# Performance work log

Hardware: AMD Instinct MI355X
Metric: run time of the kernel (lower is better)

Reference implementation:

```python
import jax, jax.numpy as jnp
import numpy as np

WS = 8            # window size
N = WS * WS       # tokens per window
C = 192           # in_features
H = 6             # heads
HD = C // H       # head dim
MH = 256          # meta network hidden
BW = 4096         # batch_size * windows
NW_MASK = 64      # number of mask window patterns


def _relative_coords_log():
    idx = np.arange(WS)
    coords = np.stack(np.meshgrid(idx, idx, indexing='ij'), axis=0).reshape(2, -1)  # [2, N]
    rel = coords[:, :, None] - coords[:, None, :]            # [2, N, N]
    rel = rel.transpose(1, 2, 0).reshape(-1, 2).astype(np.float32)  # [N*N, 2]
    return jnp.asarray(np.sign(rel) * np.log1p(np.abs(rel)))


def setup_inputs() -> dict:
    key = jax.random.key(0)
    ks = jax.random.split(key, 12)
    s = 0.02
    return {
        'x': jax.random.normal(ks[0], (BW, C, WS, WS), jnp.float32),
        'mask': jax.random.normal(ks[1], (NW_MASK, N, N), jnp.float32),
        'W_qkv': jax.random.normal(ks[2], (C, 3 * C), jnp.float32) * s,
        'b_qkv': jnp.zeros((3 * C,), jnp.float32),
        'W_proj': jax.random.normal(ks[3], (C, C), jnp.float32) * s,
        'b_proj': jnp.zeros((C,), jnp.float32),
        'mW1': jax.random.normal(ks[4], (2, MH), jnp.float32) * 0.1,
        'mb1': jnp.zeros((MH,), jnp.float32),
        'mW2': jax.random.normal(ks[5], (MH, H), jnp.float32) * 0.1,
        'mb2': jnp.zeros((H,), jnp.float32),
        'tau': jnp.ones((H,), jnp.float32),
    }


def _l2norm(v):
    n = jnp.sqrt(jnp.sum(v * v, axis=-1, keepdims=True))
    return v / jnp.maximum(n, 1e-12)


def reference(x, mask, W_qkv, b_qkv, W_proj, b_proj, mW1, mb1, mW2, mb2, tau):
    Bw = x.shape[0]
    # [Bw, C, ws, ws] -> tokens [Bw, N, C]
    tokens = x.reshape(Bw, C, N).transpose(0, 2, 1)
    qkv = tokens @ W_qkv + b_qkv                                  # [Bw, N, 3C]
    qkv = qkv.reshape(Bw, N, 3, H, HD).transpose(2, 0, 3, 1, 4)   # [3, Bw, H, N, HD]
    q, k, v = qkv[0], qkv[1], qkv[2]
    # scaled cosine attention
    attn = jnp.einsum('bhnd,bhmd->bhnm', _l2norm(q), _l2norm(k))
    attn = attn / jnp.clip(tau, 0.01, None)[None, :, None, None]
    # continuous relative position bias via meta network
    rel_log = _relative_coords_log()                              # [N*N, 2]
    bias = jax.nn.relu(rel_log @ mW1 + mb1) @ mW2 + mb2           # [N*N, H]
    bias = bias.T.reshape(H, N, N)
    attn = attn + bias[None]
    # shifted-window mask, pattern indexed by window id modulo nW_mask
    idx = jnp.arange(Bw) % mask.shape[0]
    attn = attn + mask[idx][:, None]                              # [Bw, 1, N, N]
    attn = jax.nn.softmax(attn, axis=-1)
    out = jnp.einsum('bhnm,bhmd->bhnd', attn, v)
    out = out.transpose(0, 2, 1, 3).reshape(Bw, N, C)
    out = out @ W_proj + b_proj
    # back to [Bw, C, ws, ws]
    return out.transpose(0, 2, 1).reshape(Bw, C, WS, WS)
```

## Files before the change

kernel.cpp:

```cpp
#include <hip/hip_runtime.h>

typedef _Float16 f16;
typedef _Float16 f16x2 __attribute__((ext_vector_type(2)));
typedef _Float16 f16x4 __attribute__((ext_vector_type(4)));
typedef _Float16 f16x8 __attribute__((ext_vector_type(8)));
typedef float f32x4 __attribute__((ext_vector_type(4)));

#define NT 64
#define CH 192
#define NH 6
#define MH 256
#define BWIN 4096
#define LOG2E 1.44269504f

#define STOK 200
#define SMEM_FUSED 49152

#define MFMA16(a, b, c) __builtin_amdgcn_mfma_f32_16x16x16f16(a, b, c, 0, 0, 0)
#define MFMA32(a, b, c) __builtin_amdgcn_mfma_f32_16x16x32_f16(a, b, c, 0, 0, 0)

__device__ __forceinline__ int qkidx(int n, int d) {
    return n * 32 + ((((d >> 3) + (n >> 1)) & 3) << 3) + (d & 7);
}

__global__ void bias_kernel(const float* __restrict__ mW1, const float* __restrict__ mb1,
                            const float* __restrict__ mW2, const float* __restrict__ mb2,
                            float* __restrict__ bias_tbl) {
    int p = blockIdx.x * blockDim.x + threadIdx.x;
    if (p >= NT * NT) return;
    int n = p >> 6, m = p & 63;
    float di = (float)((n >> 3) - (m >> 3));
    float dj = (float)((n & 7) - (m & 7));
    float r0 = copysignf(log1pf(fabsf(di)), di);
    float r1 = copysignf(log1pf(fabsf(dj)), dj);
    float acc[NH];
#pragma unroll
    for (int h = 0; h < NH; h++) acc[h] = mb2[h];
    for (int k = 0; k < MH; k++) {
        float hv = fmaxf(r0 * mW1[k] + r1 * mW1[MH + k] + mb1[k], 0.0f);
#pragma unroll
        for (int h = 0; h < NH; h++) acc[h] += hv * mW2[k * NH + h];
    }
#pragma unroll
    for (int h = 0; h < NH; h++) bias_tbl[h * (NT * NT) + p] = acc[h];
}

__global__ void prep_kernel(const float* __restrict__ Wqkv, const float* __restrict__ Wproj,
                            f16* __restrict__ Wpk, f16* __restrict__ Wpp) {
    int i = blockIdx.x * blockDim.x + threadIdx.x;
    const int NQ = 36 * 6 * 64 * 8;
    if (i < NQ) {
        int t = i & 7, lane = (i >> 3) & 63, ks = (i >> 9) % 6, ct = i >> 9; ct /= 6;
        int o = 16 * ct + (lane & 15);
        int c = ks * 32 + (lane >> 4) * 8 + t;
        Wpk[i] = (f16)Wqkv[c * 576 + o];
    } else if (i < NQ + 12 * 6 * 64 * 8) {
        int j = i - NQ;
        int t = j & 7, lane = (j >> 3) & 63, ks = (j >> 9) % 6, ct = j >> 9; ct /= 6;
        int o = 16 * ct + (lane & 15);
        int c = ks * 32 + (lane >> 4) * 8 + t;
        Wpp[j] = (f16)Wproj[c * 192 + o];
    }
}

__global__ void comb_kernel(const float* __restrict__ mask, const float* __restrict__ bias_tbl,
                            float* __restrict__ comb) {
    int j = blockIdx.x * blockDim.x + threadIdx.x;
    if (j >= 64 * NH * NT * NT) return;
    int im = j / (NH * NT * NT);
    int rem = j % (NH * NT * NT);
    int h = rem >> 12;
    int p = rem & 4095;
    comb[j] = (mask[im * 4096 + p] + bias_tbl[h * 4096 + p]) * LOG2E;
}

__launch_bounds__(384, 1)
__global__ void qkv_kernel(const float* __restrict__ x, const float* __restrict__ bqkv,
                           const f16* __restrict__ Wpk, f16* __restrict__ qkv_ws) {
    __shared__ __align__(16) f16 tok[NT * STOK];

    const int tid = threadIdx.x;
    const int l   = tid & 63;
    const int w   = __builtin_amdgcn_readfirstlane(tid >> 6);
    const int b   = blockIdx.x;
    const int c16 = l & 15;
    const int g4  = l >> 4;

    {
        const float* xb = x + (size_t)b * (CH * NT);
        const int n4 = 4 * c16;
#pragma unroll
        for (int i = 0; i < 4; i++) {
            int c = 32 * w + 8 * g4 + 2 * i;
            f32x4 a0 = *(const f32x4*)(xb + c * NT + n4);
            f32x4 a1 = *(const f32x4*)(xb + (c + 1) * NT + n4);
#pragma unroll
            for (int j = 0; j < 4; j++) {
                f16x2 p;
                p[0] = (f16)a0[j];
                p[1] = (f16)a1[j];
                *(f16x2*)(tok + (n4 + j) * STOK + c) = p;
            }
        }
    }
    __syncthreads();

    f16* dstq = qkv_ws + (size_t)(b * NH + w) * 6144;
    f16* dstk = dstq + 2048;
    f16* dstv = dstq + 4096;

    {
        f16x8 wf[6][2];
#pragma unroll
        for (int ks = 0; ks < 6; ks++)
#pragma unroll
            for (int dt = 0; dt < 2; dt++)
                wf[ks][dt] = *(const f16x8*)(Wpk + (((size_t)(2 * w + dt) * 6 + ks) * 64 + l) * 8);
        f32x4 acc[2][4] = {};
#pragma unroll
        for (int ks = 0; ks < 6; ks++) {
            f16x8 af[4];
#pragma unroll
            for (int nt = 0; nt < 4; nt++)
                af[nt] = *(const f16x8*)(tok + (16 * nt + c16) * STOK + ks * 32 + 8 * g4);
#pragma unroll
            for (int dt = 0; dt < 2; dt++)
#pragma unroll
                for (int nt = 0; nt < 4; nt++)
                    acc[dt][nt] = MFMA32(wf[ks][dt], af[nt], acc[dt][nt]);
        }
        f32x4 bb0 = *(const f32x4*)(bqkv + 32 * w + 4 * g4);
        f32x4 bb1 = *(const f32x4*)(bqkv + 32 * w + 16 + 4 * g4);
#pragma unroll
        for (int nt = 0; nt < 4; nt++) {
            float a0[4], a1[4];
            float ss = 0.f;
#pragma unroll
            for (int r = 0; r < 4; r++) {
                a0[r] = acc[0][nt][r] + bb0[r];
                a1[r] = acc[1][nt][r] + bb1[r];
                ss += a0[r] * a0[r] + a1[r] * a1[r];
            }
            ss += __shfl_xor(ss, 16);
            ss += __shfl_xor(ss, 32);
            float inv = 1.0f / fmaxf(sqrtf(ss), 1e-12f);
            f16x4 h0, h1;
#pragma unroll
            for (int r = 0; r < 4; r++) {
                h0[r] = (f16)(a0[r] * inv);
                h1[r] = (f16)(a1[r] * inv);
            }
            *(f16x4*)(dstq + (16 * nt + c16) * 32 + 4 * g4)      = h0;
            *(f16x4*)(dstq + (16 * nt + c16) * 32 + 16 + 4 * g4) = h1;
        }
    }
    {
        f16x8 wf[6][2];
#pragma unroll
        for (int ks = 0; ks < 6; ks++)
#pragma unroll
            for (int dt = 0; dt < 2; dt++)
                wf[ks][dt] = *(const f16x8*)(Wpk + (((size_t)(12 + 2 * w + dt) * 6 + ks) * 64 + l) * 8);
        f32x4 acc[2][4] = {};
#pragma unroll
        for (int ks = 0; ks < 6; ks++) {
            f16x8 af[4];
#pragma unroll
            for (int nt = 0; nt < 4; nt++)
                af[nt] = *(const f16x8*)(tok + (16 * nt + c16) * STOK + ks * 32 + 8 * g4);
#pragma unroll
            for (int dt = 0; dt < 2; dt++)
#pragma unroll
                for (int nt = 0; nt < 4; nt++)
                    acc[dt][nt] = MFMA32(wf[ks][dt], af[nt], acc[dt][nt]);
        }
        f32x4 bb0 = *(const f32x4*)(bqkv + CH + 32 * w + 4 * g4);
        f32x4 bb1 = *(const f32x4*)(bqkv + CH + 32 * w + 16 + 4 * g4);
#pragma unroll
        for (int nt = 0; nt < 4; nt++) {
            float a0[4], a1[4];
            float ss = 0.f;
#pragma unroll
            for (int r = 0; r < 4; r++) {
                a0[r] = acc[0][nt][r] + bb0[r];
                a1[r] = acc[1][nt][r] + bb1[r];
                ss += a0[r] * a0[r] + a1[r] * a1[r];
            }
            ss += __shfl_xor(ss, 16);
            ss += __shfl_xor(ss, 32);
            float inv = 1.0f / fmaxf(sqrtf(ss), 1e-12f);
            f16x4 h0, h1;
#pragma unroll
            for (int r = 0; r < 4; r++) {
                h0[r] = (f16)(a0[r] * inv);
                h1[r] = (f16)(a1[r] * inv);
            }
            *(f16x4*)(dstk + (16 * nt + c16) * 32 + 4 * g4)      = h0;
            *(f16x4*)(dstk + (16 * nt + c16) * 32 + 16 + 4 * g4) = h1;
        }
    }
    {
        f16x8 wf[6][2];
#pragma unroll
        for (int ks = 0; ks < 6; ks++)
#pragma unroll
            for (int dt = 0; dt < 2; dt++)
                wf[ks][dt] = *(const f16x8*)(Wpk + (((size_t)(24 + 2 * w + dt) * 6 + ks) * 64 + l) * 8);
        f32x4 acc[2][4] = {};
#pragma unroll
        for (int ks = 0; ks < 6; ks++) {
            f16x8 af[4];
#pragma unroll
            for (int mt = 0; mt < 4; mt++)
                af[mt] = *(const f16x8*)(tok + (16 * mt + c16) * STOK + ks * 32 + 8 * g4);
#pragma unroll
            for (int dt = 0; dt < 2; dt++)
#pragma unroll
                for (int mt = 0; mt < 4; mt++)
                    acc[dt][mt] = MFMA32(af[mt], wf[ks][dt], acc[dt][mt]);
        }
#pragma unroll
        for (int dt = 0; dt < 2; dt++) {
            float bb = bqkv[384 + 32 * w + 16 * dt + c16];
#pragma unroll
            for (int mt = 0; mt < 4; mt++) {
                f16x4 h;
#pragma unroll
                for (int r = 0; r < 4; r++) h[r] = (f16)(acc[dt][mt][r] + bb);
                *(f16x4*)(dstv + ((dt * 4 + mt) * 64 + l) * 4) = h;
            }
        }
    }
}

__launch_bounds__(384, 1)
__global__ void attn2_kernel(const float* __restrict__ tau, const f16* __restrict__ Wpp,
                             const float* __restrict__ bproj, const float* __restrict__ comb,
                             const f16* __restrict__ qkv_ws, float* __restrict__ out) {
    __shared__ __align__(16) f16 ao[NT * STOK];

    const int tid = threadIdx.x;
    const int l   = tid & 63;
    const int w   = __builtin_amdgcn_readfirstlane(tid >> 6);
    const int b   = blockIdx.x;
    const int c16 = l & 15;
    const int g4  = l >> 4;

    const f16* qg = qkv_ws + (size_t)(b * NH + w) * 6144;
    const f16* kg = qg + 2048;
    const f16* vg = qg + 4096;

    f16x4 vb[2][4];
#pragma unroll
    for (int dt = 0; dt < 2; dt++)
#pragma unroll
        for (int mk = 0; mk < 4; mk++)
            vb[dt][mk] = *(const f16x4*)(vg + ((dt * 4 + mk) * 64 + l) * 4);
    f16x8 wpp[6][2];
#pragma unroll
    for (int ks = 0; ks < 6; ks++)
#pragma unroll
        for (int c2 = 0; c2 < 2; c2++)
            wpp[ks][c2] = *(const f16x8*)(Wpp + (((size_t)(2 * w + c2) * 6 + ks) * 64 + l) * 8);

    const float itau_l2 = LOG2E / fmaxf(tau[w], 0.01f);
    const float* cb = comb + ((size_t)((b & 63) * NH + w)) * (NT * NT);

#pragma unroll
    for (int half = 0; half < 2; half++) {
        f32x4 cc[4][2];
#pragma unroll
        for (int mt = 0; mt < 4; mt++)
#pragma unroll
            for (int ntl = 0; ntl < 2; ntl++)
                cc[mt][ntl] = *(const f32x4*)(cb + (16 * (2 * half + ntl) + c16) * NT + 16 * mt + 4 * g4);

        f16x8 aqf[2];
#pragma unroll
        for (int ntl = 0; ntl < 2; ntl++)
            aqf[ntl] = *(const f16x8*)(qg + (16 * (2 * half + ntl) + c16) * 32 + 8 * g4);
        f16x8 akf[4];
#pragma unroll
        for (int mt = 0; mt < 4; mt++)
            akf[mt] = *(const f16x8*)(kg + (16 * mt + c16) * 32 + 8 * g4);

        f32x4 sv[4][2];
#pragma unroll
        for (int mt = 0; mt < 4; mt++)
#pragma unroll
            for (int ntl = 0; ntl < 2; ntl++) {
                f32x4 z = {};
                sv[mt][ntl] = MFMA32(akf[mt], aqf[ntl], z);
            }
#pragma unroll
        for (int mt = 0; mt < 4; mt++)
#pragma unroll
            for (int ntl = 0; ntl < 2; ntl++)
#pragma unroll
                for (int r = 0; r < 4; r++)
                    sv[mt][ntl][r] = sv[mt][ntl][r] * itau_l2 + cc[mt][ntl][r];
#pragma unroll
        for (int ntl = 0; ntl < 2; ntl++) {
            float mx = sv[0][ntl][0];
#pragma unroll
            for (int mt = 0; mt < 4; mt++)
#pragma unroll
                for (int r = 0; r < 4; r++) mx = fmaxf(mx, sv[mt][ntl][r]);
            mx = fmaxf(mx, __shfl_xor(mx, 16));
            mx = fmaxf(mx, __shfl_xor(mx, 32));
            float sum = 0.f;
#pragma unroll
            for (int mt = 0; mt < 4; mt++)
#pragma unroll
                for (int r = 0; r < 4; r++) {
                    float p = exp2f(sv[mt][ntl][r] - mx);
                    sv[mt][ntl][r] = p;
                    sum += p;
                }
            sum += __shfl_xor(sum, 16);
            sum += __shfl_xor(sum, 32);
            float ris = 1.0f / sum;
#pragma unroll
            for (int mt = 0; mt < 4; mt++)
#pragma unroll
                for (int r = 0; r < 4; r++) sv[mt][ntl][r] *= ris;
        }
        f16x4 pa[4][2];
#pragma unroll
        for (int mk = 0; mk < 4; mk++)
#pragma unroll
            for (int ntl = 0; ntl < 2; ntl++) {
                f16x4 h;
#pragma unroll
                for (int r = 0; r < 4; r++) h[r] = (f16)sv[mk][ntl][r];
                pa[mk][ntl] = h;
            }
        f32x4 av[2][2] = {};
#pragma unroll
        for (int mk = 0; mk < 4; mk++)
#pragma unroll
            for (int ntl = 0; ntl < 2; ntl++)
#pragma unroll
                for (int dt = 0; dt < 2; dt++)
                    av[ntl][dt] = MFMA16(pa[mk][ntl], vb[dt][mk], av[ntl][dt]);
#pragma unroll
        for (int ntl = 0; ntl < 2; ntl++)
#pragma unroll
            for (int dt = 0; dt < 2; dt++)
#pragma unroll
                for (int r = 0; r < 4; r++)
                    ao[(16 * (2 * half + ntl) + 4 * g4 + r) * STOK + 32 * w + 16 * dt + c16] =
                        (f16)av[ntl][dt][r];
    }
    __syncthreads();

    f32x4 acc2[2][4] = {};
#pragma unroll
    for (int ks = 0; ks < 6; ks++) {
        f16x8 af[4];
#pragma unroll
        for (int rt = 0; rt < 4; rt++)
            af[rt] = *(const f16x8*)(ao + (16 * rt + c16) * STOK + ks * 32 + 8 * g4);
#pragma unroll
        for (int c2 = 0; c2 < 2; c2++)
#pragma unroll
            for (int rt = 0; rt < 4; rt++)
                acc2[c2][rt] = MFMA32(af[rt], wpp[ks][c2], acc2[c2][rt]);
    }
    float* ob = out + (size_t)b * (CH * NT);
#pragma unroll
    for (int c2 = 0; c2 < 2; c2++) {
        int c = 16 * (2 * w + c2) + c16;
        float bp = bproj[c];
#pragma unroll
        for (int rt = 0; rt < 4; rt++) {
            f32x4 o4 = acc2[c2][rt];
            o4[0] += bp; o4[1] += bp; o4[2] += bp; o4[3] += bp;
            *(f32x4*)(ob + c * NT + 16 * rt + 4 * g4) = o4;
        }
    }
}

__launch_bounds__(384)
__global__ void attn_fused_kernel(const float* __restrict__ x, const float* __restrict__ bqkv,
                                  const float* __restrict__ bproj, const float* __restrict__ tau,
                                  const f16* __restrict__ Wpk, const f16* __restrict__ Wpp,
                                  const float* __restrict__ comb, float* __restrict__ out) {
    __shared__ __align__(16) char smem[SMEM_FUSED];
    f16* tok = (f16*)smem;
    f16* qk  = (f16*)smem;
    f16* ao  = (f16*)smem;

    const int b   = blockIdx.x;
    const int tid = threadIdx.x;
    const int l   = tid & 63;
    const int w   = __builtin_amdgcn_readfirstlane(tid >> 6);
    const int c16 = l & 15;
    const int g4  = l >> 4;

    {
        const float* xb = x + (size_t)b * (CH * NT);
        const int n4 = 4 * c16;
#pragma unroll
        for (int i = 0; i < 4; i++) {
            int c = 32 * w + 8 * g4 + 2 * i;
            f32x4 a0 = *(const f32x4*)(xb + c * NT + n4);
            f32x4 a1 = *(const f32x4*)(xb + (c + 1) * NT + n4);
#pragma unroll
            for (int j = 0; j < 4; j++) {
                f16x2 p;
                p[0] = (f16)a0[j];
                p[1] = (f16)a1[j];
                *(f16x2*)(tok + (n4 + j) * STOK + c) = p;
            }
        }
    }
    __syncthreads();

    f16x4 hq[2][4], hk[2][4];
    {
        f32x4 aq_[2][4] = {};
#pragma unroll
        for (int ks = 0; ks < 6; ks++) {
            f16x8 af[4];
#pragma unroll
            for (int nt = 0; nt < 4; nt++)
                af[nt] = *(const f16x8*)(tok + (16 * nt + c16) * STOK + ks * 32 + 8 * g4);
#pragma unroll
            for (int dt = 0; dt < 2; dt++) {
                f16x8 wf = *(const f16x8*)(Wpk + (((size_t)(2 * w + dt) * 6 + ks) * 64 + l) * 8);
#pragma unroll
                for (int nt = 0; nt < 4; nt++)
                    aq_[dt][nt] = MFMA32(wf, af[nt], aq_[dt][nt]);
            }
        }
#pragma unroll
        for (int dt = 0; dt < 2; dt++) {
            f32x4 bb = *(const f32x4*)(bqkv + 32 * w + 16 * dt + 4 * g4);
#pragma unroll
            for (int nt = 0; nt < 4; nt++)
#pragma unroll
                for (int r = 0; r < 4; r++) aq_[dt][nt][r] += bb[r];
        }
#pragma unroll
        for (int nt = 0; nt < 4; nt++) {
            float ss = 0.f;
#pragma unroll
            for (int dt = 0; dt < 2; dt++)
#pragma unroll
                for (int r = 0; r < 4; r++) ss += aq_[dt][nt][r] * aq_[dt][nt][r];
            ss += __shfl_xor(ss, 16);
            ss += __shfl_xor(ss, 32);
            float iq = 1.0f / fmaxf(sqrtf(ss), 1e-12f);
#pragma unroll
            for (int dt = 0; dt < 2; dt++)
#pragma unroll
                for (int r = 0; r < 4; r++) hq[dt][nt][r] = (f16)(aq_[dt][nt][r] * iq);
        }
    }
    {
        f32x4 ak_[2][4] = {};
// ... 145 lines not shown
#pragma unroll
    for (int mk = 0; mk < 4; mk++)
#pragma unroll
        for (int nt = 0; nt < 4; nt++)
#pragma unroll
            for (int dt = 0; dt < 2; dt++)
                av[nt][dt] = MFMA16(pa[mk][nt], vb[dt][mk], av[nt][dt]);

    __syncthreads();
#pragma unroll
    for (int nt = 0; nt < 4; nt++)
#pragma unroll
        for (int dt = 0; dt < 2; dt++)
#pragma unroll
            for (int r = 0; r < 4; r++)
                ao[(16 * nt + 4 * g4 + r) * STOK + 32 * w + 16 * dt + c16] = (f16)av[nt][dt][r];
    __syncthreads();

    f32x4 acc2[2][4] = {};
#pragma unroll
    for (int ks = 0; ks < 6; ks++) {
        f16x8 af[4];
#pragma unroll
        for (int rt = 0; rt < 4; rt++)
            af[rt] = *(const f16x8*)(ao + (16 * rt + c16) * STOK + ks * 32 + 8 * g4);
#pragma unroll
        for (int c2 = 0; c2 < 2; c2++) {
            f16x8 bw = *(const f16x8*)(Wpp + (((size_t)(2 * w + c2) * 6 + ks) * 64 + l) * 8);
#pragma unroll
            for (int rt = 0; rt < 4; rt++)
                acc2[c2][rt] = MFMA32(af[rt], bw, acc2[c2][rt]);
        }
    }
    float* ob = out + (size_t)b * (CH * NT);
#pragma unroll
    for (int c2 = 0; c2 < 2; c2++) {
        int c = 16 * (2 * w + c2) + c16;
        float bp = bproj[c];
#pragma unroll
        for (int rt = 0; rt < 4; rt++) {
            f32x4 o4 = acc2[c2][rt];
            o4[0] += bp; o4[1] += bp; o4[2] += bp; o4[3] += bp;
            *(f32x4*)(ob + c * NT + 16 * rt + 4 * g4) = o4;
        }
    }
}

#define WS_BIAS 0
#define WS_WPK  98304
#define WS_WPP  319488
#define WS_COMB 393216
#define WS_QKV  6684672
#define WS_NEED ((size_t)WS_QKV + (size_t)BWIN * NH * 6144 * 2)

extern "C" void kernel_launch(void* const* d_in, const int* in_sizes, int n_in,
                              void* d_out, int out_size, void* d_ws, size_t ws_size,
                              hipStream_t stream) {
    const float* x     = (const float*)d_in[0];
    const float* mask  = (const float*)d_in[1];
    const float* Wqkv  = (const float*)d_in[2];
    const float* bqkv  = (const float*)d_in[3];
    const float* Wproj = (const float*)d_in[4];
    const float* bproj = (const float*)d_in[5];
    const float* mW1   = (const float*)d_in[6];
    const float* mb1   = (const float*)d_in[7];
    const float* mW2   = (const float*)d_in[8];
    const float* mb2   = (const float*)d_in[9];
    const float* tau   = (const float*)d_in[10];

    char* ws = (char*)d_ws;
    float* bias_tbl = (float*)(ws + WS_BIAS);
    f16*   Wpk      = (f16*)(ws + WS_WPK);
    f16*   Wpp      = (f16*)(ws + WS_WPP);
    float* comb     = (float*)(ws + WS_COMB);
    f16*   qkv_ws   = (f16*)(ws + WS_QKV);

    bias_kernel<<<16, 256, 0, stream>>>(mW1, mb1, mW2, mb2, bias_tbl);
    int prep_n = 36 * 6 * 64 * 8 + 12 * 6 * 64 * 8;
    prep_kernel<<<(prep_n + 255) / 256, 256, 0, stream>>>(Wqkv, Wproj, Wpk, Wpp);
    int comb_n = 64 * NH * NT * NT;
    comb_kernel<<<(comb_n + 255) / 256, 256, 0, stream>>>(mask, bias_tbl, comb);

    if (ws_size >= WS_NEED) {
        qkv_kernel<<<BWIN, 384, 0, stream>>>(x, bqkv, Wpk, qkv_ws);
        attn2_kernel<<<BWIN, 384, 0, stream>>>(tau, Wpp, bproj, comb, qkv_ws, (float*)d_out);
    } else {
        attn_fused_kernel<<<BWIN, 384, 0, stream>>>(x, bqkv, bproj, tau, Wpk, Wpp, comb,
                                                    (float*)d_out);
    }
}
```

Before: 314.5 us.

## Stage weights and QKV tiles through LDS with async global-to-LDS loads

Replaces per-lane register preloads of the packed QKV and projection weights and the per-window q/k/v tiles with asynchronous global_load_lds transfers into shared-memory staging buffers. In the QKV kernel the next weight slice is prefetched during each epilogue, and q/k are written with an XOR swizzle that the attention kernel reads back. V is now stored in wider 8-element vectors, and the attention output staging buffer reuses the q/k/v staging area after a barrier. This is meant to cut register pressure and overlap weight fetch with compute, at the cost of a much larger shared-memory footprint that may limit occupancy, plus hand-placed wait counters.

```diff
diff --git a/kernel.cpp b/kernel.cpp
--- a/kernel.cpp
+++ b/kernel.cpp
@@ -18,6 +18,16 @@
 
 #define MFMA16(a, b, c) __builtin_amdgcn_mfma_f32_16x16x16f16(a, b, c, 0, 0, 0)
 #define MFMA32(a, b, c) __builtin_amdgcn_mfma_f32_16x16x32_f16(a, b, c, 0, 0, 0)
+
+typedef const __attribute__((address_space(1))) void* gas_ptr;
+typedef __attribute__((address_space(3))) void* las_ptr;
+__device__ __forceinline__ void gload_lds16(const void* g, void* l) {
+    __builtin_amdgcn_global_load_lds((gas_ptr)g, (las_ptr)l, 16, 0, 0);
+}
+#define WAIT_VMCNT(N) do { asm volatile("s_waitcnt vmcnt(" #N ")" ::: "memory"); \
+                           __builtin_amdgcn_sched_barrier(0); } while (0)
+#define WAIT_LGKM0()  do { asm volatile("s_waitcnt lgkmcnt(0)" ::: "memory"); \
+                           __builtin_amdgcn_sched_barrier(0); } while (0)
 
 __device__ __forceinline__ int qkidx(int n, int d) {
     return n * 32 + ((((d >> 3) + (n >> 1)) & 3) << 3) + (d & 7);
@@ -78,6 +88,7 @@
 __global__ void qkv_kernel(const float* __restrict__ x, const float* __restrict__ bqkv,
                            const f16* __restrict__ Wpk, f16* __restrict__ qkv_ws) {
     __shared__ __align__(16) f16 tok[NT * STOK];
+    __shared__ __align__(16) f16 wstage[6 * 6144];
 
     const int tid = threadIdx.x;
     const int l   = tid & 63;
@@ -86,6 +97,15 @@
     const int c16 = l & 15;
     const int g4  = l >> 4;
 
+    f16* wbuf = wstage + w * 6144;
+
+    {
+        const f16* src = Wpk + (size_t)(2 * w) * 3072;
+#pragma unroll
+        for (int j = 0; j < 12; j++)
+            gload_lds16(src + j * 512 + l * 8, wbuf + j * 512);
+    }
+
     {
         const float* xb = x + (size_t)b * (CH * NT);
         const int n4 = 4 * c16;
@@ -104,31 +124,37 @@
         }
     }
     __syncthreads();
-
+    WAIT_VMCNT(0);
+
+    const int swz = ((c16 >> 1) & 3) << 3;
     f16* dstq = qkv_ws + (size_t)(b * NH + w) * 6144;
     f16* dstk = dstq + 2048;
     f16* dstv = dstq + 4096;
 
     {
-        f16x8 wf[6][2];
-#pragma unroll
-        for (int ks = 0; ks < 6; ks++)
-#pragma unroll
-            for (int dt = 0; dt < 2; dt++)
-                wf[ks][dt] = *(const f16x8*)(Wpk + (((size_t)(2 * w + dt) * 6 + ks) * 64 + l) * 8);
         f32x4 acc[2][4] = {};
 #pragma unroll
         for (int ks = 0; ks < 6; ks++) {
+            f16x8 wf0 = *(const f16x8*)(wbuf + (ks * 64 + l) * 8);
+            f16x8 wf1 = *(const f16x8*)(wbuf + ((6 + ks) * 64 + l) * 8);
             f16x8 af[4];
 #pragma unroll
             for (int nt = 0; nt < 4; nt++)
                 af[nt] = *(const f16x8*)(tok + (16 * nt + c16) * STOK + ks * 32 + 8 * g4);
 #pragma unroll
-            for (int dt = 0; dt < 2; dt++)
-#pragma unroll
-                for (int nt = 0; nt < 4; nt++)
-                    acc[dt][nt] = MFMA32(wf[ks][dt], af[nt], acc[dt][nt]);
-        }
+            for (int nt = 0; nt < 4; nt++) {
+                acc[0][nt] = MFMA32(wf0, af[nt], acc[0][nt]);
+                acc[1][nt] = MFMA32(wf1, af[nt], acc[1][nt]);
+            }
+        }
+        WAIT_LGKM0();
+        {
+            const f16* src = Wpk + (size_t)(12 + 2 * w) * 3072;
+#pragma unroll
+            for (int j = 0; j < 12; j++)
+                gload_lds16(src + j * 512 + l * 8, wbuf + j * 512);
+        }
+        __builtin_amdgcn_sched_barrier(0);
         f32x4 bb0 = *(const f32x4*)(bqkv + 32 * w + 4 * g4);
         f32x4 bb1 = *(const f32x4*)(bqkv + 32 * w + 16 + 4 * g4);
 #pragma unroll
@@ -150,30 +176,37 @@
                 h0[r] = (f16)(a0[r] * inv);
                 h1[r] = (f16)(a1[r] * inv);
             }
-            *(f16x4*)(dstq + (16 * nt + c16) * 32 + 4 * g4)      = h0;
-            *(f16x4*)(dstq + (16 * nt + c16) * 32 + 16 + 4 * g4) = h1;
-        }
-    }
-    {
-        f16x8 wf[6][2];
-#pragma unroll
-        for (int ks = 0; ks < 6; ks++)
-#pragma unroll
-            for (int dt = 0; dt < 2; dt++)
-                wf[ks][dt] = *(const f16x8*)(Wpk + (((size_t)(12 + 2 * w + dt) * 6 + ks) * 64 + l) * 8);
+            int base = (16 * nt + c16) * 32;
+            *(f16x4*)(dstq + base + ((4 * g4) ^ swz))      = h0;
+            *(f16x4*)(dstq + base + ((16 + 4 * g4) ^ swz)) = h1;
+        }
+    }
+    WAIT_VMCNT(0);
+
+    {
         f32x4 acc[2][4] = {};
 #pragma unroll
         for (int ks = 0; ks < 6; ks++) {
+            f16x8 wf0 = *(const f16x8*)(wbuf + (ks * 64 + l) * 8);
+            f16x8 wf1 = *(const f16x8*)(wbuf + ((6 + ks) * 64 + l) * 8);
             f16x8 af[4];
 #pragma unroll
             for (int nt = 0; nt < 4; nt++)
                 af[nt] = *(const f16x8*)(tok + (16 * nt + c16) * STOK + ks * 32 + 8 * g4);
 #pragma unroll
-            for (int dt = 0; dt < 2; dt++)
-#pragma unroll
-                for (int nt = 0; nt < 4; nt++)
-                    acc[dt][nt] = MFMA32(wf[ks][dt], af[nt], acc[dt][nt]);
-        }
+            for (int nt = 0; nt < 4; nt++) {
+                acc[0][nt] = MFMA32(wf0, af[nt], acc[0][nt]);
+                acc[1][nt] = MFMA32(wf1, af[nt], acc[1][nt]);
+            }
+        }
+        WAIT_LGKM0();
+        {
+            const f16* src = Wpk + (size_t)(24 + 2 * w) * 3072;
+#pragma unroll
+            for (int j = 0; j < 12; j++)
+                gload_lds16(src + j * 512 + l * 8, wbuf + j * 512);
+        }
+        __builtin_amdgcn_sched_barrier(0);
         f32x4 bb0 = *(const f32x4*)(bqkv + CH + 32 * w + 4 * g4);
         f32x4 bb1 = *(const f32x4*)(bqkv + CH + 32 * w + 16 + 4 * g4);
 #pragma unroll
@@ -195,40 +228,45 @@
                 h0[r] = (f16)(a0[r] * inv);
                 h1[r] = (f16)(a1[r] * inv);
             }
-            *(f16x4*)(dstk + (16 * nt + c16) * 32 + 4 * g4)      = h0;
-            *(f16x4*)(dstk + (16 * nt + c16) * 32 + 16 + 4 * g4) = h1;
-        }
-    }
-    {
-        f16x8 wf[6][2];
-#pragma unroll
-        for (int ks = 0; ks < 6; ks++)
-#pragma unroll
-            for (int dt = 0; dt < 2; dt++)
-                wf[ks][dt] = *(const f16x8*)(Wpk + (((size_t)(24 + 2 * w + dt) * 6 + ks) * 64 + l) * 8);
+            int base = (16 * nt + c16) * 32;
+            *(f16x4*)(dstk + base + ((4 * g4) ^ swz))      = h0;
+            *(f16x4*)(dstk + base + ((16 + 4 * g4) ^ swz)) = h1;
+        }
+    }
+    WAIT_VMCNT(0);
+
+    {
         f32x4 acc[2][4] = {};
 #pragma unroll
         for (int ks = 0; ks < 6; ks++) {
+            f16x8 wf0 = *(const f16x8*)(wbuf + (ks * 64 + l) * 8);
+            f16x8 wf1 = *(const f16x8*)(wbuf + ((6 + ks) * 64 + l) * 8);
             f16x8 af[4];
 #pragma unroll
             for (int mt = 0; mt < 4; mt++)
                 af[mt] = *(const f16x8*)(tok + (16 * mt + c16) * STOK + ks * 32 + 8 * g4);
 #pragma unroll
-            for (int dt = 0; dt < 2; dt++)
-#pragma unroll
-                for (int mt = 0; mt < 4; mt++)
-                    acc[dt][mt] = MFMA32(af[mt], wf[ks][dt], acc[dt][mt]);
-        }
+            for (int mt = 0; mt < 4; mt++) {
+                acc[0][mt] = MFMA32(af[mt], wf0, acc[0][mt]);
+                acc[1][mt] = MFMA32(af[mt], wf1, acc[1][mt]);
+            }
+        }
+        f16x4 hv[2][4];
 #pragma unroll
         for (int dt = 0; dt < 2; dt++) {
             float bb = bqkv[384 + 32 * w + 16 * dt + c16];
 #pragma unroll
-            for (int mt = 0; mt < 4; mt++) {
-                f16x4 h;
-#pragma unroll
-                for (int r = 0; r < 4; r++) h[r] = (f16)(acc[dt][mt][r] + bb);
-                *(f16x4*)(dstv + ((dt * 4 + mt) * 64 + l) * 4) = h;
-            }
+            for (int mt = 0; mt < 4; mt++)
+#pragma unroll
+                for (int r = 0; r < 4; r++) hv[dt][mt][r] = (f16)(acc[dt][mt][r] + bb);
+        }
+#pragma unroll
+        for (int p = 0; p < 4; p++) {
+            int dt = p >> 1, m0 = 2 * (p & 1);
+            f16x8 v8;
+#pragma unroll
+            for (int r = 0; r < 4; r++) { v8[r] = hv[dt][m0][r]; v8[4 + r] = hv[dt][m0 + 1][r]; }
+            *(f16x8*)(dstv + (p * 64 + l) * 8) = v8;
         }
     }
 }
@@ -237,7 +275,8 @@
 __global__ void attn2_kernel(const float* __restrict__ tau, const f16* __restrict__ Wpp,
                              const float* __restrict__ bproj, const float* __restrict__ comb,
                              const f16* __restrict__ qkv_ws, float* __restrict__ out) {
-    __shared__ __align__(16) f16 ao[NT * STOK];
+    __shared__ __align__(16) f16 qkvstage[6 * 6144];
+    __shared__ __align__(16) f16 wppstage[6 * 6144];
 
     const int tid = threadIdx.x;
     const int l   = tid & 63;
@@ -246,26 +285,37 @@
     const int c16 = l & 15;
     const int g4  = l >> 4;
 
-    const f16* qg = qkv_ws + (size_t)(b * NH + w) * 6144;
-    const f16* kg = qg + 2048;
-    const f16* vg = qg + 4096;
-
-    f16x4 vb[2][4];
-#pragma unroll
-    for (int dt = 0; dt < 2; dt++)
-#pragma unroll
-        for (int mk = 0; mk < 4; mk++)
-            vb[dt][mk] = *(const f16x4*)(vg + ((dt * 4 + mk) * 64 + l) * 4);
-    f16x8 wpp[6][2];
-#pragma unroll
-    for (int ks = 0; ks < 6; ks++)
-#pragma unroll
-        for (int c2 = 0; c2 < 2; c2++)
-            wpp[ks][c2] = *(const f16x8*)(Wpp + (((size_t)(2 * w + c2) * 6 + ks) * 64 + l) * 8);
+    f16* Lq = qkvstage + w * 6144;
+    f16* Lw = wppstage + w * 6144;
+    f16* ao = qkvstage;
+
+    {
+        const f16* srcq = qkv_ws + (size_t)(b * NH + w) * 6144;
+#pragma unroll
+        for (int j = 0; j < 12; j++)
+            gload_lds16(srcq + j * 512 + l * 8, Lq + j * 512);
+        const f16* srcw = Wpp + (size_t)(2 * w) * 3072;
+#pragma unroll
+        for (int j = 0; j < 12; j++)
+            gload_lds16(srcw + j * 512 + l * 8, Lw + j * 512);
+    }
 
     const float itau_l2 = LOG2E / fmaxf(tau[w], 0.01f);
     const float* cb = comb + ((size_t)((b & 63) * NH + w)) * (NT * NT);
-
+    const int swz = ((c16 >> 1) & 3) << 3;
+
+    WAIT_VMCNT(12);
+
+    f16x4 vb[2][4];
+#pragma unroll
+    for (int p = 0; p < 4; p++) {
+        f16x8 v8 = *(const f16x8*)(Lq + 4096 + (p * 64 + l) * 8);
+        int dt = p >> 1, m0 = 2 * (p & 1);
+#pragma unroll
+        for (int r = 0; r < 4; r++) { vb[dt][m0][r] = v8[r]; vb[dt][m0 + 1][r] = v8[4 + r]; }
+    }
+
+    f32x4 avh[2][2][2];
 #pragma unroll
     for (int half = 0; half < 2; half++) {
         f32x4 cc[4][2];
@@ -278,11 +328,11 @@
         f16x8 aqf[2];
 #pragma unroll
         for (int ntl = 0; ntl < 2; ntl++)
-            aqf[ntl] = *(const f16x8*)(qg + (16 * (2 * half + ntl) + c16) * 32 + 8 * g4);
+            aqf[ntl] = *(const f16x8*)(Lq + (16 * (2 * half + ntl) + c16) * 32 + ((8 * g4) ^ swz));
         f16x8 akf[4];
 #pragma unroll
         for (int mt = 0; mt < 4; mt++)
-            akf[mt] = *(const f16x8*)(kg + (16 * mt + c16) * 32 + 8 * g4);
+            akf[mt] = *(const f16x8*)(Lq + 2048 + (16 * mt + c16) * 32 + ((8 * g4) ^ swz));
 
         f32x4 sv[4][2];
 #pragma unroll
@@ -347,12 +397,23 @@
         for (int ntl = 0; ntl < 2; ntl++)
 #pragma unroll
             for (int dt = 0; dt < 2; dt++)
+                avh[half][ntl][dt] = av[ntl][dt];
+    }
+
+    __syncthreads();
+
+#pragma unroll
+    for (int half = 0; half < 2; half++)
+#pragma unroll
+        for (int ntl = 0; ntl < 2; ntl++)
+#pragma unroll
+            for (int dt = 0; dt < 2; dt++)
 #pragma unroll
                 for (int r = 0; r < 4; r++)
                     ao[(16 * (2 * half + ntl) + 4 * g4 + r) * STOK + 32 * w + 16 * dt + c16] =
-                        (f16)av[ntl][dt][r];
-    }
+                        (f16)avh[half][ntl][dt][r];
     __syncthreads();
+    WAIT_VMCNT(0);
 
     f32x4 acc2[2][4] = {};
 #pragma unroll
@@ -361,11 +422,13 @@
 #pragma unroll
         for (int rt = 0; rt < 4; rt++)
             af[rt] = *(const f16x8*)(ao + (16 * rt + c16) * STOK + ks * 32 + 8 * g4);
-#pragma unroll
-        for (int c2 = 0; c2 < 2; c2++)
-#pragma unroll
-            for (int rt = 0; rt < 4; rt++)
-                acc2[c2][rt] = MFMA32(af[rt], wpp[ks][c2], acc2[c2][rt]);
+        f16x8 w0 = *(const f16x8*)(Lw + (ks * 64 + l) * 8);
+        f16x8 w1 = *(const f16x8*)(Lw + ((6 + ks) * 64 + l) * 8);
+#pragma unroll
+        for (int rt = 0; rt < 4; rt++) {
+            acc2[0][rt] = MFMA32(af[rt], w0, acc2[0][rt]);
+            acc2[1][rt] = MFMA32(af[rt], w1, acc2[1][rt]);
+        }
     }
     float* ob = out + (size_t)b * (CH * NT);
 #pragma unroll
```

Measured after the change: 380.8 us. 1.21x slower.

## Process two windows per block in QKV and attention kernels

Applied to the files above, without the earlier changes.

Each block of the QKV and attention kernels now handles two windows instead of one, with doubled LDS buffers and grids halved. The weight fragments held in registers are reused across both windows, and interleaving two independent MFMA chains gives more instruction-level parallelism. The V layout is also packed into 16-byte stores and loads. The cost is roughly double register and LDS pressure per block and half as many blocks, which may reduce occupancy or cause spills.

```diff
diff --git a/kernel.cpp b/kernel.cpp
--- a/kernel.cpp
+++ b/kernel.cpp
@@ -74,40 +74,73 @@
     comb[j] = (mask[im * 4096 + p] + bias_tbl[h * 4096 + p]) * LOG2E;
 }
 
+__device__ __forceinline__ void norm_store(const f32x4 (&acc)[2][4], const float* __restrict__ bq,
+                                           int c16, int g4, f16* __restrict__ dst) {
+    f32x4 bb0 = *(const f32x4*)(bq + 4 * g4);
+    f32x4 bb1 = *(const f32x4*)(bq + 16 + 4 * g4);
+#pragma unroll
+    for (int nt = 0; nt < 4; nt++) {
+        float a0[4], a1[4];
+        float ss = 0.f;
+#pragma unroll
+        for (int r = 0; r < 4; r++) {
+            a0[r] = acc[0][nt][r] + bb0[r];
+            a1[r] = acc[1][nt][r] + bb1[r];
+            ss += a0[r] * a0[r] + a1[r] * a1[r];
+        }
+        ss += __shfl_xor(ss, 16);
+        ss += __shfl_xor(ss, 32);
+        float inv = 1.0f / fmaxf(sqrtf(ss), 1e-12f);
+        f16x4 h0, h1;
+#pragma unroll
+        for (int r = 0; r < 4; r++) {
+            h0[r] = (f16)(a0[r] * inv);
+            h1[r] = (f16)(a1[r] * inv);
+        }
+        *(f16x4*)(dst + (16 * nt + c16) * 32 + 4 * g4)      = h0;
+        *(f16x4*)(dst + (16 * nt + c16) * 32 + 16 + 4 * g4) = h1;
+    }
+}
+
 __launch_bounds__(384, 1)
 __global__ void qkv_kernel(const float* __restrict__ x, const float* __restrict__ bqkv,
                            const f16* __restrict__ Wpk, f16* __restrict__ qkv_ws) {
-    __shared__ __align__(16) f16 tok[NT * STOK];
+    __shared__ __align__(16) f16 tokA[NT * STOK];
+    __shared__ __align__(16) f16 tokB[NT * STOK];
 
     const int tid = threadIdx.x;
     const int l   = tid & 63;
     const int w   = __builtin_amdgcn_readfirstlane(tid >> 6);
-    const int b   = blockIdx.x;
+    const int b0  = blockIdx.x * 2;
+    const int b1  = b0 + 1;
     const int c16 = l & 15;
     const int g4  = l >> 4;
 
     {
-        const float* xb = x + (size_t)b * (CH * NT);
         const int n4 = 4 * c16;
 #pragma unroll
-        for (int i = 0; i < 4; i++) {
-            int c = 32 * w + 8 * g4 + 2 * i;
-            f32x4 a0 = *(const f32x4*)(xb + c * NT + n4);
-            f32x4 a1 = *(const f32x4*)(xb + (c + 1) * NT + n4);
-#pragma unroll
-            for (int j = 0; j < 4; j++) {
-                f16x2 p;
-                p[0] = (f16)a0[j];
-                p[1] = (f16)a1[j];
-                *(f16x2*)(tok + (n4 + j) * STOK + c) = p;
+        for (int wp = 0; wp < 2; wp++) {
+            const float* xb = x + (size_t)(b0 + wp) * (CH * NT);
+            f16* tok = wp ? tokB : tokA;
+#pragma unroll
+            for (int i = 0; i < 4; i++) {
+                int c = 32 * w + 8 * g4 + 2 * i;
+                f32x4 a0 = *(const f32x4*)(xb + c * NT + n4);
+                f32x4 a1 = *(const f32x4*)(xb + (c + 1) * NT + n4);
+#pragma unroll
+                for (int j = 0; j < 4; j++) {
+                    f16x2 p;
+                    p[0] = (f16)a0[j];
+                    p[1] = (f16)a1[j];
+                    *(f16x2*)(tok + (n4 + j) * STOK + c) = p;
+                }
             }
         }
     }
     __syncthreads();
 
-    f16* dstq = qkv_ws + (size_t)(b * NH + w) * 6144;
-    f16* dstk = dstq + 2048;
-    f16* dstv = dstq + 4096;
+    f16* dqA = qkv_ws + (size_t)(b0 * NH + w) * 6144;
+    f16* dqB = qkv_ws + (size_t)(b1 * NH + w) * 6144;
 
     {
         f16x8 wf[6][2];
@@ -116,43 +149,25 @@
 #pragma unroll
             for (int dt = 0; dt < 2; dt++)
                 wf[ks][dt] = *(const f16x8*)(Wpk + (((size_t)(2 * w + dt) * 6 + ks) * 64 + l) * 8);
-        f32x4 acc[2][4] = {};
+        f32x4 accA[2][4] = {}, accB[2][4] = {};
 #pragma unroll
         for (int ks = 0; ks < 6; ks++) {
-            f16x8 af[4];
-#pragma unroll
-            for (int nt = 0; nt < 4; nt++)
-                af[nt] = *(const f16x8*)(tok + (16 * nt + c16) * STOK + ks * 32 + 8 * g4);
-#pragma unroll
-            for (int dt = 0; dt < 2; dt++)
-#pragma unroll
-                for (int nt = 0; nt < 4; nt++)
-                    acc[dt][nt] = MFMA32(wf[ks][dt], af[nt], acc[dt][nt]);
-        }
-        f32x4 bb0 = *(const f32x4*)(bqkv + 32 * w + 4 * g4);
-        f32x4 bb1 = *(const f32x4*)(bqkv + 32 * w + 16 + 4 * g4);
-#pragma unroll
-        for (int nt = 0; nt < 4; nt++) {
-            float a0[4], a1[4];
-            float ss = 0.f;
-#pragma unroll
-            for (int r = 0; r < 4; r++) {
-                a0[r] = acc[0][nt][r] + bb0[r];
-                a1[r] = acc[1][nt][r] + bb1[r];
-                ss += a0[r] * a0[r] + a1[r] * a1[r];
-            }
-            ss += __shfl_xor(ss, 16);
-            ss += __shfl_xor(ss, 32);
-            float inv = 1.0f / fmaxf(sqrtf(ss), 1e-12f);
-            f16x4 h0, h1;
-#pragma unroll
-            for (int r = 0; r < 4; r++) {
-                h0[r] = (f16)(a0[r] * inv);
-                h1[r] = (f16)(a1[r] * inv);
-            }
-            *(f16x4*)(dstq + (16 * nt + c16) * 32 + 4 * g4)      = h0;
-            *(f16x4*)(dstq + (16 * nt + c16) * 32 + 16 + 4 * g4) = h1;
-        }
+            f16x8 afA[4], afB[4];
+#pragma unroll
+            for (int nt = 0; nt < 4; nt++) {
+                afA[nt] = *(const f16x8*)(tokA + (16 * nt + c16) * STOK + ks * 32 + 8 * g4);
+                afB[nt] = *(const f16x8*)(tokB + (16 * nt + c16) * STOK + ks * 32 + 8 * g4);
+            }
+#pragma unroll
+            for (int dt = 0; dt < 2; dt++)
+#pragma unroll
+                for (int nt = 0; nt < 4; nt++) {
+                    accA[dt][nt] = MFMA32(wf[ks][dt], afA[nt], accA[dt][nt]);
+                    accB[dt][nt] = MFMA32(wf[ks][dt], afB[nt], accB[dt][nt]);
+                }
+        }
+        norm_store(accA, bqkv + 32 * w, c16, g4, dqA);
+        norm_store(accB, bqkv + 32 * w, c16, g4, dqB);
     }
     {
         f16x8 wf[6][2];
@@ -161,43 +176,25 @@
 #pragma unroll
             for (int dt = 0; dt < 2; dt++)
                 wf[ks][dt] = *(const f16x8*)(Wpk + (((size_t)(12 + 2 * w + dt) * 6 + ks) * 64 + l) * 8);
-        f32x4 acc[2][4] = {};
+        f32x4 accA[2][4] = {}, accB[2][4] = {};
 #pragma unroll
         for (int ks = 0; ks < 6; ks++) {
-            f16x8 af[4];
-#pragma unroll
-            for (int nt = 0; nt < 4; nt++)
-                af[nt] = *(const f16x8*)(tok + (16 * nt + c16) * STOK + ks * 32 + 8 * g4);
-#pragma unroll
-            for (int dt = 0; dt < 2; dt++)
-#pragma unroll
-                for (int nt = 0; nt < 4; nt++)
-                    acc[dt][nt] = MFMA32(wf[ks][dt], af[nt], acc[dt][nt]);
-        }
-        f32x4 bb0 = *(const f32x4*)(bqkv + CH + 32 * w + 4 * g4);
-        f32x4 bb1 = *(const f32x4*)(bqkv + CH + 32 * w + 16 + 4 * g4);
-#pragma unroll
-        for (int nt = 0; nt < 4; nt++) {
-            float a0[4], a1[4];
-            float ss = 0.f;
-#pragma unroll
-            for (int r = 0; r < 4; r++) {
-                a0[r] = acc[0][nt][r] + bb0[r];
-                a1[r] = acc[1][nt][r] + bb1[r];
-                ss += a0[r] * a0[r] + a1[r] * a1[r];
-            }
-            ss += __shfl_xor(ss, 16);
-            ss += __shfl_xor(ss, 32);
-            float inv = 1.0f / fmaxf(sqrtf(ss), 1e-12f);
-            f16x4 h0, h1;
-#pragma unroll
-            for (int r = 0; r < 4; r++) {
-                h0[r] = (f16)(a0[r] * inv);
-                h1[r] = (f16)(a1[r] * inv);
-            }
-            *(f16x4*)(dstk + (16 * nt + c16) * 32 + 4 * g4)      = h0;
-            *(f16x4*)(dstk + (16 * nt + c16) * 32 + 16 + 4 * g4) = h1;
-        }
+            f16x8 afA[4], afB[4];
+#pragma unroll
+            for (int nt = 0; nt < 4; nt++) {
+                afA[nt] = *(const f16x8*)(tokA + (16 * nt + c16) * STOK + ks * 32 + 8 * g4);
+                afB[nt] = *(const f16x8*)(tokB + (16 * nt + c16) * STOK + ks * 32 + 8 * g4);
+            }
+#pragma unroll
+            for (int dt = 0; dt < 2; dt++)
+#pragma unroll
+                for (int nt = 0; nt < 4; nt++) {
+                    accA[dt][nt] = MFMA32(wf[ks][dt], afA[nt], accA[dt][nt]);
+                    accB[dt][nt] = MFMA32(wf[ks][dt], afB[nt], accB[dt][nt]);
+                }
+        }
+        norm_store(accA, bqkv + CH + 32 * w, c16, g4, dqA + 2048);
+        norm_store(accB, bqkv + CH + 32 * w, c16, g4, dqB + 2048);
     }
     {
         f16x8 wf[6][2];
@@ -206,28 +203,43 @@
 #pragma unroll
             for (int dt = 0; dt < 2; dt++)
                 wf[ks][dt] = *(const f16x8*)(Wpk + (((size_t)(24 + 2 * w + dt) * 6 + ks) * 64 + l) * 8);
-        f32x4 acc[2][4] = {};
+        f32x4 accA[2][4] = {}, accB[2][4] = {};
 #pragma unroll
         for (int ks = 0; ks < 6; ks++) {
-            f16x8 af[4];
-#pragma unroll
-            for (int mt = 0; mt < 4; mt++)
-                af[mt] = *(const f16x8*)(tok + (16 * mt + c16) * STOK + ks * 32 + 8 * g4);
-#pragma unroll
-            for (int dt = 0; dt < 2; dt++)
+            f16x8 afA[4], afB[4];
+#pragma unroll
+            for (int mt = 0; mt < 4; mt++) {
+                afA[mt] = *(const f16x8*)(tokA + (16 * mt + c16) * STOK + ks * 32 + 8 * g4);
+                afB[mt] = *(const f16x8*)(tokB + (16 * mt + c16) * STOK + ks * 32 + 8 * g4);
+            }
+#pragma unroll
+            for (int dt = 0; dt < 2; dt++)
+#pragma unroll
+                for (int mt = 0; mt < 4; mt++) {
+                    accA[dt][mt] = MFMA32(afA[mt], wf[ks][dt], accA[dt][mt]);
+                    accB[dt][mt] = MFMA32(afB[mt], wf[ks][dt], accB[dt][mt]);
+                }
+        }
+#pragma unroll
+        for (int wp = 0; wp < 2; wp++) {
+            f16* dstv = (wp ? dqB : dqA) + 4096;
+            f16x4 hv[2][4];
+#pragma unroll
+            for (int dt = 0; dt < 2; dt++) {
+                float bb = bqkv[384 + 32 * w + 16 * dt + c16];
 #pragma unroll
                 for (int mt = 0; mt < 4; mt++)
-                    acc[dt][mt] = MFMA32(af[mt], wf[ks][dt], acc[dt][mt]);
-        }
-#pragma unroll
-        for (int dt = 0; dt < 2; dt++) {
-            float bb = bqkv[384 + 32 * w + 16 * dt + c16];
-#pragma unroll
-            for (int mt = 0; mt < 4; mt++) {
-                f16x4 h;
-#pragma unroll
-                for (int r = 0; r < 4; r++) h[r] = (f16)(acc[dt][mt][r] + bb);
-                *(f16x4*)(dstv + ((dt * 4 + mt) * 64 + l) * 4) = h;
+#pragma unroll
+                    for (int r = 0; r < 4; r++)
+                        hv[dt][mt][r] = (f16)((wp ? accB : accA)[dt][mt][r] + bb);
+            }
+#pragma unroll
+            for (int p = 0; p < 4; p++) {
+                int dt = p >> 1, m0 = 2 * (p & 1);
+                f16x8 v8;
+#pragma unroll
+                for (int r = 0; r < 4; r++) { v8[r] = hv[dt][m0][r]; v8[4 + r] = hv[dt][m0 + 1][r]; }
+                *(f16x8*)(dstv + (p * 64 + l) * 8) = v8;
             }
         }
     }
@@ -237,146 +249,182 @@
 __global__ void attn2_kernel(const float* __restrict__ tau, const f16* __restrict__ Wpp,
                              const float* __restrict__ bproj, const float* __restrict__ comb,
                              const f16* __restrict__ qkv_ws, float* __restrict__ out) {
-    __shared__ __align__(16) f16 ao[NT * STOK];
+    __shared__ __align__(16) f16 aoA[NT * STOK];
+    __shared__ __align__(16) f16 aoB[NT * STOK];
 
     const int tid = threadIdx.x;
     const int l   = tid & 63;
     const int w   = __builtin_amdgcn_readfirstlane(tid >> 6);
-    const int b   = blockIdx.x;
+    const int b0  = blockIdx.x * 2;
+    const int b1  = b0 + 1;
     const int c16 = l & 15;
     const int g4  = l >> 4;
 
-    const f16* qg = qkv_ws + (size_t)(b * NH + w) * 6144;
-    const f16* kg = qg + 2048;
-    const f16* vg = qg + 4096;
-
-    f16x4 vb[2][4];
-#pragma unroll
-    for (int dt = 0; dt < 2; dt++)
+    const f16* qgA = qkv_ws + (size_t)(b0 * NH + w) * 6144;
+    const f16* qgB = qkv_ws + (size_t)(b1 * NH + w) * 6144;
+
+    f16x4 vbA[2][4], vbB[2][4];
+#pragma unroll
+    for (int p = 0; p < 4; p++) {
+        f16x8 vA = *(const f16x8*)(qgA + 4096 + (p * 64 + l) * 8);
+        f16x8 vB = *(const f16x8*)(qgB + 4096 + (p * 64 + l) * 8);
+        int dt = p >> 1, m0 = 2 * (p & 1);
+#pragma unroll
+        for (int r = 0; r < 4; r++) {
+            vbA[dt][m0][r] = vA[r]; vbA[dt][m0 + 1][r] = vA[4 + r];
+            vbB[dt][m0][r] = vB[r]; vbB[dt][m0 + 1][r] = vB[4 + r];
+        }
+    }
+
+    const float itau_l2 = LOG2E / fmaxf(tau[w], 0.01f);
+    const float* cbA = comb + ((size_t)((b0 & 63) * NH + w)) * (NT * NT);
+    const float* cbB = comb + ((size_t)((b1 & 63) * NH + w)) * (NT * NT);
+
+#pragma unroll
+    for (int half = 0; half < 2; half++) {
+        f16x8 aqfA[2], aqfB[2], akfA[4], akfB[4];
+#pragma unroll
+        for (int ntl = 0; ntl < 2; ntl++) {
+            aqfA[ntl] = *(const f16x8*)(qgA + (16 * (2 * half + ntl) + c16) * 32 + 8 * g4);
+            aqfB[ntl] = *(const f16x8*)(qgB + (16 * (2 * half + ntl) + c16) * 32 + 8 * g4);
+        }
+#pragma unroll
+        for (int mt = 0; mt < 4; mt++) {
+            akfA[mt] = *(const f16x8*)(qgA + 2048 + (16 * mt + c16) * 32 + 8 * g4);
+            akfB[mt] = *(const f16x8*)(qgB + 2048 + (16 * mt + c16) * 32 + 8 * g4);
+        }
+
+        f32x4 svA[4][2], svB[4][2];
+#pragma unroll
+        for (int mt = 0; mt < 4; mt++)
+#pragma unroll
+            for (int ntl = 0; ntl < 2; ntl++) {
+                f32x4 z = {};
+                svA[mt][ntl] = MFMA32(akfA[mt], aqfA[ntl], z);
+                f32x4 z2 = {};
+                svB[mt][ntl] = MFMA32(akfB[mt], aqfB[ntl], z2);
+            }
+#pragma unroll
+        for (int mt = 0; mt < 4; mt++)
+#pragma unroll
+            for (int ntl = 0; ntl < 2; ntl++) {
+                int nt = 2 * half + ntl;
+                f32x4 cA = *(const f32x4*)(cbA + (16 * nt + c16) * NT + 16 * mt + 4 * g4);
+                f32x4 cB = *(const f32x4*)(cbB + (16 * nt + c16) * NT + 16 * mt + 4 * g4);
+#pragma unroll
+                for (int r = 0; r < 4; r++) {
+                    svA[mt][ntl][r] = svA[mt][ntl][r] * itau_l2 + cA[r];
+                    svB[mt][ntl][r] = svB[mt][ntl][r] * itau_l2 + cB[r];
+                }
+            }
+#pragma unroll
+        for (int ntl = 0; ntl < 2; ntl++) {
+            float mxA = svA[0][ntl][0], mxB = svB[0][ntl][0];
+#pragma unroll
+            for (int mt = 0; mt < 4; mt++)
+#pragma unroll
+                for (int r = 0; r < 4; r++) {
+                    mxA = fmaxf(mxA, svA[mt][ntl][r]);
+                    mxB = fmaxf(mxB, svB[mt][ntl][r]);
+                }
+            mxA = fmaxf(mxA, __shfl_xor(mxA, 16));
+            mxA = fmaxf(mxA, __shfl_xor(mxA, 32));
+            mxB = fmaxf(mxB, __shfl_xor(mxB, 16));
+            mxB = fmaxf(mxB, __shfl_xor(mxB, 32));
+            float sumA = 0.f, sumB = 0.f;
+#pragma unroll
+            for (int mt = 0; mt < 4; mt++)
+#pragma unroll
+                for (int r = 0; r < 4; r++) {
+                    float pA = exp2f(svA[mt][ntl][r] - mxA);
+                    float pB = exp2f(svB[mt][ntl][r] - mxB);
+                    svA[mt][ntl][r] = pA; sumA += pA;
+                    svB[mt][ntl][r] = pB; sumB += pB;
+                }
+            sumA += __shfl_xor(sumA, 16);
+            sumA += __shfl_xor(sumA, 32);
+            sumB += __shfl_xor(sumB, 16);
+            sumB += __shfl_xor(sumB, 32);
+            float risA = 1.0f / sumA, risB = 1.0f / sumB;
+#pragma unroll
+            for (int mt = 0; mt < 4; mt++)
+#pragma unroll
+                for (int r = 0; r < 4; r++) {
+                    svA[mt][ntl][r] *= risA;
+                    svB[mt][ntl][r] *= risB;
+                }
+        }
+        f16x4 paA[4][2], paB[4][2];
 #pragma unroll
         for (int mk = 0; mk < 4; mk++)
-            vb[dt][mk] = *(const f16x4*)(vg + ((dt * 4 + mk) * 64 + l) * 4);
+#pragma unroll
+            for (int ntl = 0; ntl < 2; ntl++) {
+                f16x4 hA, hB;
+#pragma unroll
+                for (int r = 0; r < 4; r++) { hA[r] = (f16)svA[mk][ntl][r]; hB[r] = (f16)svB[mk][ntl][r]; }
+                paA[mk][ntl] = hA;
+                paB[mk][ntl] = hB;
+            }
+        f32x4 avA[2][2] = {}, avB[2][2] = {};
+#pragma unroll
+        for (int mk = 0; mk < 4; mk++)
+#pragma unroll
+            for (int ntl = 0; ntl < 2; ntl++)
+#pragma unroll
+                for (int dt = 0; dt < 2; dt++) {
+                    avA[ntl][dt] = MFMA16(paA[mk][ntl], vbA[dt][mk], avA[ntl][dt]);
+                    avB[ntl][dt] = MFMA16(paB[mk][ntl], vbB[dt][mk], avB[ntl][dt]);
+                }
+#pragma unroll
+        for (int ntl = 0; ntl < 2; ntl++)
+#pragma unroll
+            for (int dt = 0; dt < 2; dt++)
+#pragma unroll
+                for (int r = 0; r < 4; r++) {
+                    int row = (16 * (2 * half + ntl) + 4 * g4 + r) * STOK + 32 * w + 16 * dt + c16;
+                    aoA[row] = (f16)avA[ntl][dt][r];
+                    aoB[row] = (f16)avB[ntl][dt][r];
+                }
+    }
+    __syncthreads();
+
     f16x8 wpp[6][2];
 #pragma unroll
     for (int ks = 0; ks < 6; ks++)
 #pragma unroll
         for (int c2 = 0; c2 < 2; c2++)
             wpp[ks][c2] = *(const f16x8*)(Wpp + (((size_t)(2 * w + c2) * 6 + ks) * 64 + l) * 8);
-
-    const float itau_l2 = LOG2E / fmaxf(tau[w], 0.01f);
-    const float* cb = comb + ((size_t)((b & 63) * NH + w)) * (NT * NT);
-
-#pragma unroll
-    for (int half = 0; half < 2; half++) {
-        f32x4 cc[4][2];
-#pragma unroll
-        for (int mt = 0; mt < 4; mt++)
-#pragma unroll
-            for (int ntl = 0; ntl < 2; ntl++)
-                cc[mt][ntl] = *(const f32x4*)(cb + (16 * (2 * half + ntl) + c16) * NT + 16 * mt + 4 * g4);
-
-        f16x8 aqf[2];
-#pragma unroll
-        for (int ntl = 0; ntl < 2; ntl++)
-            aqf[ntl] = *(const f16x8*)(qg + (16 * (2 * half + ntl) + c16) * 32 + 8 * g4);
-        f16x8 akf[4];
-#pragma unroll
-        for (int mt = 0; mt < 4; mt++)
-            akf[mt] = *(const f16x8*)(kg + (16 * mt + c16) * 32 + 8 * g4);
-
-        f32x4 sv[4][2];
-#pragma unroll
-        for (int mt = 0; mt < 4; mt++)
-#pragma unroll
-            for (int ntl = 0; ntl < 2; ntl++) {
-                f32x4 z = {};
-                sv[mt][ntl] = MFMA32(akf[mt], aqf[ntl], z);
-            }
-#pragma unroll
-        for (int mt = 0; mt < 4; mt++)
-#pragma unroll
-            for (int ntl = 0; ntl < 2; ntl++)
-#pragma unroll
-                for (int r = 0; r < 4; r++)
-                    sv[mt][ntl][r] = sv[mt][ntl][r] * itau_l2 + cc[mt][ntl][r];
-#pragma unroll
-        for (int ntl = 0; ntl < 2; ntl++) {
-            float mx = sv[0][ntl][0];
-#pragma unroll
-            for (int mt = 0; mt < 4; mt++)
-#pragma unroll
-                for (int r = 0; r < 4; r++) mx = fmaxf(mx, sv[mt][ntl][r]);
-            mx = fmaxf(mx, __shfl_xor(mx, 16));
-            mx = fmaxf(mx, __shfl_xor(mx, 32));
-            float sum = 0.f;
-#pragma unroll
-            for (int mt = 0; mt < 4; mt++)
-#pragma unroll
-                for (int r = 0; r < 4; r++) {
-                    float p = exp2f(sv[mt][ntl][r] - mx);
-                    sv[mt][ntl][r] = p;
-                    sum += p;
-                }
-            sum += __shfl_xor(sum, 16);
-            sum += __shfl_xor(sum, 32);
-            float ris = 1.0f / sum;
-#pragma unroll
-            for (int mt = 0; mt < 4; mt++)
-#pragma unroll
-                for (int r = 0; r < 4; r++) sv[mt][ntl][r] *= ris;
-        }
-        f16x4 pa[4][2];
-#pragma unroll
-        for (int mk = 0; mk < 4; mk++)
-#pragma unroll
-            for (int ntl = 0; ntl < 2; ntl++) {
-                f16x4 h;
-#pragma unroll
-                for (int r = 0; r < 4; r++) h[r] = (f16)sv[mk][ntl][r];
-                pa[mk][ntl] = h;
-            }
-        f32x4 av[2][2] = {};
-#pragma unroll
-        for (int mk = 0; mk < 4; mk++)
-#pragma unroll
-            for (int ntl = 0; ntl < 2; ntl++)
-#pragma unroll
-                for (int dt = 0; dt < 2; dt++)
-                    av[ntl][dt] = MFMA16(pa[mk][ntl], vb[dt][mk], av[ntl][dt]);
-#pragma unroll
-        for (int ntl = 0; ntl < 2; ntl++)
-#pragma unroll
-            for (int dt = 0; dt < 2; dt++)
-#pragma unroll
-                for (int r = 0; r < 4; r++)
-                    ao[(16 * (2 * half + ntl) + 4 * g4 + r) * STOK + 32 * w + 16 * dt + c16] =
-                        (f16)av[ntl][dt][r];
-    }
-    __syncthreads();
-
-    f32x4 acc2[2][4] = {};
+    f32x4 accA[2][4] = {}, accB[2][4] = {};
 #pragma unroll
     for (int ks = 0; ks < 6; ks++) {
-        f16x8 af[4];
-#pragma unroll
-        for (int rt = 0; rt < 4; rt++)
-            af[rt] = *(const f16x8*)(ao + (16 * rt + c16) * STOK + ks * 32 + 8 * g4);
+        f16x8 afA[4], afB[4];
+#pragma unroll
+        for (int rt = 0; rt < 4; rt++) {
+            afA[rt] = *(const f16x8*)(aoA + (16 * rt + c16) * STOK + ks * 32 + 8 * g4);
+            afB[rt] = *(const f16x8*)(aoB + (16 * rt + c16) * STOK + ks * 32 + 8 * g4);
+        }
 #pragma unroll
         for (int c2 = 0; c2 < 2; c2++)
 #pragma unroll
-            for (int rt = 0; rt < 4; rt++)
-                acc2[c2][rt] = MFMA32(af[rt], wpp[ks][c2], acc2[c2][rt]);
-    }
-    float* ob = out + (size_t)b * (CH * NT);
+            for (int rt = 0; rt < 4; rt++) {
+                accA[c2][rt] = MFMA32(afA[rt], wpp[ks][c2], accA[c2][rt]);
+                accB[c2][rt] = MFMA32(afB[rt], wpp[ks][c2], accB[c2][rt]);
+            }
+    }
+    float* obA = out + (size_t)b0 * (CH * NT);
+    float* obB = out + (size_t)b1 * (CH * NT);
 #pragma unroll
     for (int c2 = 0; c2 < 2; c2++) {
         int c = 16 * (2 * w + c2) + c16;
         float bp = bproj[c];
 #pragma unroll
         for (int rt = 0; rt < 4; rt++) {
-            f32x4 o4 = acc2[c2][rt];
-            o4[0] += bp; o4[1] += bp; o4[2] += bp; o4[3] += bp;
-            *(f32x4*)(ob + c * NT + 16 * rt + 4 * g4) = o4;
+            f32x4 oA = accA[c2][rt];
+            f32x4 oB = accB[c2][rt];
+#pragma unroll
+            for (int r = 0; r < 4; r++) { oA[r] += bp; oB[r] += bp; }
+            *(f32x4*)(obA + c * NT + 16 * rt + 4 * g4) = oA;
+            *(f32x4*)(obB + c * NT + 16 * rt + 4 * g4) = oB;
         }
     }
 }
@@ -688,8 +736,8 @@
     comb_kernel<<<(comb_n + 255) / 256, 256, 0, stream>>>(mask, bias_tbl, comb);
 
     if (ws_size >= WS_NEED) {
-        qkv_kernel<<<BWIN, 384, 0, stream>>>(x, bqkv, Wpk, qkv_ws);
-        attn2_kernel<<<BWIN, 384, 0, stream>>>(tau, Wpp, bproj, comb, qkv_ws, (float*)d_out);
+        qkv_kernel<<<BWIN / 2, 384, 0, stream>>>(x, bqkv, Wpk, qkv_ws);
+        attn2_kernel<<<BWIN / 2, 384, 0, stream>>>(tau, Wpp, bproj, comb, qkv_ws, (float*)d_out);
     } else {
         attn_fused_kernel<<<BWIN, 384, 0, stream>>>(x, bqkv, bproj, tau, Wpk, Wpp, comb,
                                                     (float*)d_out);
```

Result: slower. 380.9 us (+21.1%).
